# Kernel optimization log

Hardware: AMD Instinct MI355X
Metric: run time of the kernel (lower is better)

The kernel has to match this reference:

```python
import jax, jax.numpy as jnp
import numpy as np

GAMMA = 1.4
N_PTS, N_IC, HID = 32768, 16384, 128


def _mlp(layers, p):
    # tanh MLP; layers = list of (W, b), last layer linear
    h = p
    for W, b in layers[:-1]:
        h = jnp.tanh(h @ W + b)
    W, b = layers[-1]
    return h @ W + b


def setup_inputs() -> dict:
    key = jax.random.key(0)
    ks = jax.random.split(key, 16)
    d = {
        "x_train": jax.random.uniform(ks[0], (N_PTS, 3), jnp.float32),
        "x_initial": jax.random.uniform(ks[1], (N_IC, 3), jnp.float32),
        "ic": jax.random.uniform(ks[2], (4, 4), jnp.float32),
    }
    def lin(k, fi, fo):
        return jax.random.normal(k, (fi, fo), jnp.float32) * np.float32(np.sqrt(1.0 / fi))
    dims_m = [(3, HID), (HID, HID), (HID, HID), (HID, 4)]
    dims_n = [(3, HID), (HID, HID), (HID, HID), (HID, 1)]
    for i, (fi, fo) in enumerate(dims_m):
        d[f"mw{i}"] = lin(ks[3 + i], fi, fo)
        d[f"mb{i}"] = jnp.zeros((fo,), jnp.float32)
    for i, (fi, fo) in enumerate(dims_n):
        d[f"nw{i}"] = lin(ks[8 + i], fi, fo)
        d[f"nb{i}"] = jnp.zeros((fo,), jnp.float32)
    return d


def _loss(x_train, x_initial, ic,
          mw0, mb0, mw1, mb1, mw2, mb2, mw3, mb3,
          nw0, nb0, nw1, nb1, nw2, nb2, nw3, nb3):
    layers_m = [(mw0, mb0), (mw1, mb1), (mw2, mb2), (mw3, mb3)]
    layers_n = [(nw0, nb0), (nw1, nb1), (nw2, nb2), (nw3, nb3)]

    def prim(p):  # p: (3,) = (x, y, t)
        o = _mlp(layers_m, p)
        rho, pr, u, v = o[0], o[1], o[2], o[3]
        E = pr / (GAMMA - 1.0) + 0.5 * rho * (u * u + v * v)
        return rho, pr, u, v, E

    def Ufn(p):  # conserved state U1..U4
        rho, pr, u, v, E = prim(p)
        return jnp.stack([rho, rho * u, rho * v, E])

    def quant(p):  # [U1..U4, f1..f4, g1..g4]
        rho, pr, u, v, E = prim(p)
        U = jnp.stack([rho, rho * u, rho * v, E])
        f = jnp.stack([rho * u, rho * u * u + pr, rho * u * v, u * (E + pr)])
        g = jnp.stack([rho * v, rho * u * v, rho * v * v + pr, v * (E + pr)])
        return jnp.concatenate([U, f, g])

    # one fused forward-mode Jacobian sweep replaces 20 torch autograd.grad calls
    J = jax.vmap(jax.jacfwd(quant))(x_train)            # (N, 12, 3)
    Hs = jax.vmap(jax.jacfwd(jax.jacfwd(Ufn)))(x_train)  # (N, 4, 3, 3)

    mu = 0.01 * jnp.squeeze(_mlp(layers_n, x_train), -1) ** 2  # (N,)
    lap = Hs[:, :, 0, 0] + Hs[:, :, 1, 1]               # U_xx + U_yy, (N, 4)
    # res_i = U_i_t + f_i_x + g_i_y - mu * (U_i_xx + U_i_yy)
    res = J[:, 0:4, 2] + J[:, 4:8, 0] + J[:, 8:12, 1] - mu[:, None] * lap
    r = jnp.mean(res ** 2, axis=0)                      # (4,) -> r1..r4

    # initial-condition quadrant loss (masked means, jit-safe)
    pred = _mlp(layers_m, x_initial)                    # (Ni, 4)
    xl = x_initial[:, 0] < 0.5
    xr = x_initial[:, 0] > 0.5
    yt = x_initial[:, 1] > 0.5
    yb = x_initial[:, 1] < 0.5
    perm = jnp.array([0, 3, 1, 2])  # ic columns -> [rho, p, u, v] target order
    init_loss = jnp.float32(0.0)
    for row, mask in ((1, xl & yt), (3, xr & yt), (0, xl & yb), (2, xr & yb)):
        tgt = ic[row][perm]                             # (4,)
        m = mask.astype(pred.dtype)
        denom = jnp.maximum(jnp.sum(m), 1.0)
        init_loss = init_loss + jnp.sum(m[:, None] * (pred - tgt) ** 2) / denom

    return jnp.sum(r) + 10.0 * init_loss + 0.1 * jnp.mean(mu ** 2)


def reference(x_train, x_initial, ic,
              mw0, mb0, mw1, mb1, mw2, mb2, mw3, mb3,
              nw0, nb0, nw1, nb1, nw2, nb2, nw3, nb3):
    return _loss(x_train, x_initial, ic,
                 mw0, mb0, mw1, mb1, mw2, mb2, mw3, mb3,
                 nw0, nb0, nw1, nb1, nw2, nb2, nw3, nb3)
```

## Files before the change

kernel.cpp:

```cpp
#include <hip/hip_runtime.h>

#define NPTS 32768
#define NIC  16384
#define GRID 256
#define BLK  512
#define NW   8

typedef __attribute__((ext_vector_type(8))) _Float16 f16x8;
typedef __attribute__((ext_vector_type(4))) float f32x4;

#define SWZ(e, r) ((e) ^ (((r) & 7) << 3))
#define MFMA16 __builtin_amdgcn_mfma_f32_16x16x32_f16

__device__ __forceinline__ float tanh_fast(float x) {
    float e = __expf(2.0f * x);
    return 1.0f - 2.0f / (e + 1.0f);
}

__device__ __forceinline__ float wave_allsum(float v) {
#pragma unroll
    for (int off = 32; off > 0; off >>= 1) v += __shfl_xor(v, off, 64);
    return v;
}

__device__ __forceinline__ unsigned short f2hb(float x) {
    return __builtin_bit_cast(unsigned short, (_Float16)x);
}
__device__ __forceinline__ uint2 pack4h(float a, float b, float c, float d) {
    return make_uint2((unsigned)f2hb(a) | ((unsigned)f2hb(b) << 16),
                      (unsigned)f2hb(c) | ((unsigned)f2hb(d) << 16));
}

__global__ __launch_bounds__(BLK) void k_prep(
    const float* __restrict__ mw1, const float* __restrict__ mw2,
    const float* __restrict__ nw1, const float* __restrict__ nw2,
    const float* __restrict__ mw3,
    unsigned short* __restrict__ wt1, unsigned short* __restrict__ wt2,
    unsigned short* __restrict__ nt1, unsigned short* __restrict__ nt2,
    unsigned short* __restrict__ w3t) {
    const int tid = threadIdx.x;
    const int bk = blockIdx.x;
    if (bk == 4) {
        for (int i = tid; i < 2048; i += BLK) w3t[i] = 0;
        __syncthreads();
        if (tid < 512) {
            const int j = tid & 127, k = tid >> 7;
            w3t[k * 128 + SWZ(j, k)] = f2hb(mw3[j * 4 + k]);
        }
        return;
    }
    const float* src = (bk == 0) ? mw1 : (bk == 1) ? mw2 : (bk == 2) ? nw1 : nw2;
    unsigned short* dst = (bk == 0) ? wt1 : (bk == 1) ? wt2 : (bk == 2) ? nt1 : nt2;
    __shared__ float sM[128 * 129];
#pragma unroll
    for (int k = 0; k < 32; k++) {
        const int idx = tid + k * BLK;
        const int j = idx >> 7, n = idx & 127;
        sM[n * 129 + j] = src[idx];
    }
    __syncthreads();
#pragma unroll
    for (int k = 0; k < 32; k++) {
        const int d = tid + k * BLK;
        const int n = d >> 7, js = d & 127;
        const int j = js ^ ((n & 7) << 3);
        dst[d] = f2hb(sM[n * 129 + j]);
    }
}

__global__ __launch_bounds__(BLK) void k_fused(
    const float* __restrict__ xtr, const float* __restrict__ xin,
    const float* __restrict__ icg,
    const float* __restrict__ mw0, const float* __restrict__ mb0,
    const float* __restrict__ mb1, const float* __restrict__ mb2,
    const float* __restrict__ mw3, const float* __restrict__ mb3,
    const float* __restrict__ nw0, const float* __restrict__ nb0,
    const float* __restrict__ nb1, const float* __restrict__ nb2,
    const float* __restrict__ nw3, const float* __restrict__ nb3,
    const unsigned short* __restrict__ wt1, const unsigned short* __restrict__ wt2,
    const unsigned short* __restrict__ nt1, const unsigned short* __restrict__ nt2,
    const unsigned short* __restrict__ w3t,
    float* __restrict__ resPart, float* __restrict__ muPart,
    float* __restrict__ icPart) {
    __shared__ __align__(16) _Float16 sW1[16384];
    __shared__ __align__(16) _Float16 sW2[16384];
    __shared__ __align__(16) _Float16 sH[6 * 4096];
    __shared__ __align__(16) _Float16 sW3[2048];
    __shared__ __align__(16) float sO[768];
    __shared__ float sB[520];
    __shared__ float sV[128];
    __shared__ float sW3v[512];
    __shared__ float sMu[128];
    __shared__ float sTq[16];
    __shared__ float sRed[NW][8];

    const int tid = threadIdx.x;
    const int lane = tid & 63, wv = tid >> 6;
    const int g = lane >> 4, l15 = lane & 15;
    const int rtp = wv >> 1, ptile = wv & 1;
    const int bp = ptile * 16 + l15;
    const int p32 = tid & 31;
    const int chunk = tid >> 5;
    const int base = blockIdx.x * 128;

    {
        const uint4* s4 = (const uint4*)nt1;
        uint4* d4 = (uint4*)sW1;
#pragma unroll
        for (int k = 0; k < 4; k++) d4[tid + k * BLK] = s4[tid + k * BLK];
        s4 = (const uint4*)nt2; d4 = (uint4*)sW2;
#pragma unroll
        for (int k = 0; k < 4; k++) d4[tid + k * BLK] = s4[tid + k * BLK];
        if (tid < 128) {
            sV[tid] = nw3[tid];
            sB[260 + tid] = nb1[tid];
            sB[388 + tid] = nb2[tid];
        }
        if (tid == 0) sB[516] = nb3[0];
    }
    float wxr[8], wyr[8], wzr[8], wbr[8];
#pragma unroll
    for (int j = 0; j < 8; j++) {
        const int n = chunk * 8 + j;
        wxr[j] = nw0[n]; wyr[j] = nw0[128 + n]; wzr[j] = nw0[256 + n]; wbr[j] = nb0[n];
    }
    __syncthreads();

    float accMu2 = 0.f;
    for (int b = 0; b < 4; b++) {
        const int pt0 = base + b * 32;
        {
            const int p = pt0 + p32;
            const float x = xtr[p * 3 + 0], y = xtr[p * 3 + 1], t = xtr[p * 3 + 2];
            float hv[8];
#pragma unroll
            for (int j = 0; j < 8; j++)
                hv[j] = tanh_fast(fmaf(wxr[j], x, fmaf(wyr[j], y, fmaf(wzr[j], t, wbr[j]))));
            const uint2 lo = pack4h(hv[0], hv[1], hv[2], hv[3]);
            const uint2 hi = pack4h(hv[4], hv[5], hv[6], hv[7]);
            *(uint4*)&sH[p32 * 128 + SWZ(chunk * 8, p32)] = make_uint4(lo.x, lo.y, hi.x, hi.y);
        }
        __syncthreads();
#pragma unroll
        for (int L = 0; L < 2; L++) {
            const _Float16* W = (L == 0) ? sW1 : sW2;
            f32x4 a0 = (f32x4){0.f, 0.f, 0.f, 0.f};
            f32x4 a1 = (f32x4){0.f, 0.f, 0.f, 0.f};
#pragma unroll
            for (int ks = 0; ks < 4; ks++) {
                const int ee = SWZ(ks * 32 + g * 8, l15);
                const f16x8 A0 = *(const f16x8*)&W[(rtp * 32 + l15) * 128 + ee];
                const f16x8 A1 = *(const f16x8*)&W[(rtp * 32 + 16 + l15) * 128 + ee];
                const f16x8 Bv = *(const f16x8*)&sH[bp * 128 + ee];
                a0 = MFMA16(A0, Bv, a0, 0, 0, 0);
                a1 = MFMA16(A1, Bv, a1, 0, 0, 0);
            }
            float hv[2][4];
#pragma unroll
            for (int r = 0; r < 4; r++) {
                const int n0 = rtp * 32 + g * 4 + r;
                hv[0][r] = tanh_fast(a0[r] + sB[260 + L * 128 + n0]);
                hv[1][r] = tanh_fast(a1[r] + sB[260 + L * 128 + n0 + 16]);
            }
            __syncthreads();
#pragma unroll
            for (int rr = 0; rr < 2; rr++)
                *(uint2*)&sH[bp * 128 + SWZ(rtp * 32 + rr * 16 + g * 4, bp)] =
                    pack4h(hv[rr][0], hv[rr][1], hv[rr][2], hv[rr][3]);
            __syncthreads();
        }
#pragma unroll
        for (int q = 0; q < 4; q++) {
            const int lp = wv * 4 + q;
            const float h1 = (float)sH[lp * 128 + SWZ(lane, lp)];
            const float h2 = (float)sH[lp * 128 + SWZ(64 + lane, lp)];
            float o = fmaf(h1, sV[lane], h2 * sV[64 + lane]);
            o = wave_allsum(o) + sB[516];
            const float muv = 0.01f * o * o;
            if (lane == 0) sMu[b * 32 + lp] = muv;
            accMu2 += muv * muv;
        }
        __syncthreads();
    }
    if (lane == 0) sRed[wv][0] = accMu2;
    __syncthreads();
    if (tid == 0) {
        float s = 0.f;
#pragma unroll
        for (int w = 0; w < NW; w++) s += sRed[w][0];
        muPart[blockIdx.x] = s;
    }
    __syncthreads();

    {
        const uint4* s4 = (const uint4*)wt1;
        uint4* d4 = (uint4*)sW1;
#pragma unroll
        for (int k = 0; k < 4; k++) d4[tid + k * BLK] = s4[tid + k * BLK];
        s4 = (const uint4*)wt2; d4 = (uint4*)sW2;
#pragma unroll
        for (int k = 0; k < 4; k++) d4[tid + k * BLK] = s4[tid + k * BLK];
        if (tid < 256) ((uint4*)sW3)[tid] = ((const uint4*)w3t)[tid];
        {
            const int k = tid >> 7, j = tid & 127;
            sW3v[k * 128 + j] = mw3[j * 4 + k];
        }
        if (tid < 128) { sB[tid] = mb1[tid]; sB[128 + tid] = mb2[tid]; }
        if (tid < 4) sB[256 + tid] = mb3[tid];
        if (tid < 16) {
            const int k = tid & 3, q = tid >> 2;
            const int row = (q == 0) ? 1 : ((q == 1) ? 3 : ((q == 2) ? 0 : 2));
            const int pc = (k == 0) ? 0 : ((k == 1) ? 3 : ((k == 2) ? 1 : 2));
            sTq[q * 4 + k] = icg[row * 4 + pc];
        }
    }
#pragma unroll
    for (int j = 0; j < 8; j++) {
        const int n = chunk * 8 + j;
        wxr[j] = mw0[n]; wyr[j] = mw0[128 + n]; wzr[j] = mw0[256 + n]; wbr[j] = mb0[n];
    }
    __syncthreads();

    float qs[4] = {0, 0, 0, 0}, qc[4] = {0, 0, 0, 0};
    for (int b = 0; b < 2; b++) {
        const int pt0 = blockIdx.x * 64 + b * 32;
        {
            const int p = pt0 + p32;
            const float x = xin[p * 3 + 0], y = xin[p * 3 + 1], t = xin[p * 3 + 2];
            float hv[8];
#pragma unroll
            for (int j = 0; j < 8; j++)
                hv[j] = tanh_fast(fmaf(wxr[j], x, fmaf(wyr[j], y, fmaf(wzr[j], t, wbr[j]))));
            const uint2 lo = pack4h(hv[0], hv[1], hv[2], hv[3]);
            const uint2 hi = pack4h(hv[4], hv[5], hv[6], hv[7]);
            *(uint4*)&sH[p32 * 128 + SWZ(chunk * 8, p32)] = make_uint4(lo.x, lo.y, hi.x, hi.y);
        }
        __syncthreads();
#pragma unroll
        for (int L = 0; L < 2; L++) {
            const _Float16* W = (L == 0) ? sW1 : sW2;
            f32x4 a0 = (f32x4){0.f, 0.f, 0.f, 0.f};
            f32x4 a1 = (f32x4){0.f, 0.f, 0.f, 0.f};
#pragma unroll
            for (int ks = 0; ks < 4; ks++) {
                const int ee = SWZ(ks * 32 + g * 8, l15);
                const f16x8 A0 = *(const f16x8*)&W[(rtp * 32 + l15) * 128 + ee];
                const f16x8 A1 = *(const f16x8*)&W[(rtp * 32 + 16 + l15) * 128 + ee];
                const f16x8 Bv = *(const f16x8*)&sH[bp * 128 + ee];
                a0 = MFMA16(A0, Bv, a0, 0, 0, 0);
                a1 = MFMA16(A1, Bv, a1, 0, 0, 0);
            }
            float hv[2][4];
#pragma unroll
            for (int r = 0; r < 4; r++) {
                const int n0 = rtp * 32 + g * 4 + r;
                hv[0][r] = tanh_fast(a0[r] + sB[L * 128 + n0]);
                hv[1][r] = tanh_fast(a1[r] + sB[L * 128 + n0 + 16]);
            }
            __syncthreads();
#pragma unroll
            for (int rr = 0; rr < 2; rr++)
                *(uint2*)&sH[bp * 128 + SWZ(rtp * 32 + rr * 16 + g * 4, bp)] =
                    pack4h(hv[rr][0], hv[rr][1], hv[rr][2], hv[rr][3]);
            __syncthreads();
        }
#pragma unroll
        for (int q = 0; q < 4; q++) {
            const int lp = wv * 4 + q;
            const int p = pt0 + lp;
            const float h1 = (float)sH[lp * 128 + SWZ(lane, lp)];
            const float h2 = (float)sH[lp * 128 + SWZ(64 + lane, lp)];
            float o0 = fmaf(h1, sW3v[lane], h2 * sW3v[64 + lane]);
            float o1 = fmaf(h1, sW3v[128 + lane], h2 * sW3v[192 + lane]);
            float o2 = fmaf(h1, sW3v[256 + lane], h2 * sW3v[320 + lane]);
            float o3 = fmaf(h1, sW3v[384 + lane], h2 * sW3v[448 + lane]);
            o0 = wave_allsum(o0) + sB[256];
            o1 = wave_allsum(o1) + sB[257];
            o2 = wave_allsum(o2) + sB[258];
            o3 = wave_allsum(o3) + sB[259];

            const float x = xin[p * 3 + 0];
            const float y = xin[p * 3 + 1];
            int quad = -1;
            if (x < 0.5f && y > 0.5f) quad = 0;
            else if (x > 0.5f && y > 0.5f) quad = 1;
            else if (x < 0.5f && y < 0.5f) quad = 2;
            else if (x > 0.5f && y < 0.5f) quad = 3;
            if (quad >= 0) {
                const float d0 = o0 - sTq[quad * 4 + 0];
                const float d1 = o1 - sTq[quad * 4 + 1];
                const float d2 = o2 - sTq[quad * 4 + 2];
                const float d3 = o3 - sTq[quad * 4 + 3];
                const float ss = d0 * d0 + d1 * d1 + d2 * d2 + d3 * d3;
#pragma unroll
                for (int qq = 0; qq < 4; qq++) {
                    qs[qq] += (quad == qq) ? ss : 0.f;
                    qc[qq] += (quad == qq) ? 1.f : 0.f;
                }
            }
        }
        __syncthreads();
    }
    if (lane == 0) {
#pragma unroll
        for (int q = 0; q < 4; q++) { sRed[wv][q] = qs[q]; sRed[wv][4 + q] = qc[q]; }
    }
    __syncthreads();
    if (tid == 0) {
        float s[8] = {0, 0, 0, 0, 0, 0, 0, 0};
#pragma unroll
        for (int w = 0; w < NW; w++)
#pragma unroll
            for (int q = 0; q < 8; q++) s[q] += sRed[w][q];
#pragma unroll
        for (int q = 0; q < 8; q++) icPart[blockIdx.x * 8 + q] = s[q];
    }
    __syncthreads();

    float racc0 = 0.f, racc1 = 0.f, racc2 = 0.f, racc3 = 0.f;
    for (int b = 0; b < 4; b++) {
        const int pt0 = base + b * 32;

        {
            const int p = pt0 + p32;
            const float x = xtr[p * 3 + 0], y = xtr[p * 3 + 1], t = xtr[p * 3 + 2];
            float ch[6][8];
#pragma unroll
            for (int j = 0; j < 8; j++) {
                const float z = fmaf(wxr[j], x, fmaf(wyr[j], y, fmaf(wzr[j], t, wbr[j])));
                const float a = tanh_fast(z);
                const float s = 1.f - a * a;
                ch[0][j] = a;
                ch[1][j] = s * wxr[j];
                ch[2][j] = s * wyr[j];
                ch[3][j] = s * wzr[j];
                ch[4][j] = -2.f * a * s * wxr[j] * wxr[j];
                ch[5][j] = -2.f * a * s * wyr[j] * wyr[j];
            }
            const int off = p32 * 128 + SWZ(chunk * 8, p32);
#pragma unroll
            for (int c = 0; c < 6; c++) {
                const uint2 lo = pack4h(ch[c][0], ch[c][1], ch[c][2], ch[c][3]);
                const uint2 hi = pack4h(ch[c][4], ch[c][5], ch[c][6], ch[c][7]);
                *(uint4*)&sH[c * 4096 + off] = make_uint4(lo.x, lo.y, hi.x, hi.y);
            }
        }
        __syncthreads();

#pragma unroll
        for (int L = 0; L < 2; L++) {
            const _Float16* W = (L == 0) ? sW1 : sW2;
            f32x4 acc[2][6];
#pragma unroll
            for (int rr = 0; rr < 2; rr++)
#pragma unroll
                for (int c = 0; c < 6; c++) acc[rr][c] = (f32x4){0.f, 0.f, 0.f, 0.f};
#pragma unroll
            for (int ks = 0; ks < 4; ks++) {
                const int ee = SWZ(ks * 32 + g * 8, l15);
                const f16x8 A0 = *(const f16x8*)&W[(rtp * 32 + l15) * 128 + ee];
                const f16x8 A1 = *(const f16x8*)&W[(rtp * 32 + 16 + l15) * 128 + ee];
#pragma unroll
                for (int c = 0; c < 6; c++) {
                    const f16x8 Bv = *(const f16x8*)&sH[c * 4096 + bp * 128 + ee];
                    acc[0][c] = MFMA16(A0, Bv, acc[0][c], 0, 0, 0);
                    acc[1][c] = MFMA16(A1, Bv, acc[1][c], 0, 0, 0);
                }
            }
            float ch[2][6][4];
#pragma unroll
            for (int rr = 0; rr < 2; rr++)
#pragma unroll
                for (int r = 0; r < 4; r++) {
                    const int n = rtp * 32 + rr * 16 + g * 4 + r;
                    const float z0 = acc[rr][0][r] + sB[L * 128 + n];
                    const float a = tanh_fast(z0);
                    const float s = 1.f - a * a;
                    const float zx = acc[rr][1][r], zy = acc[rr][2][r];
                    ch[rr][0][r] = a;
                    ch[rr][1][r] = s * zx;
                    ch[rr][2][r] = s * zy;
                    ch[rr][3][r] = s * acc[rr][3][r];
                    ch[rr][4][r] = s * acc[rr][4][r] - 2.f * a * s * zx * zx;
                    ch[rr][5][r] = s * acc[rr][5][r] - 2.f * a * s * zy * zy;
                }
            __syncthreads();
#pragma unroll
            for (int rr = 0; rr < 2; rr++) {
                const int eo = bp * 128 + SWZ(rtp * 32 + rr * 16 + g * 4, bp);
#pragma unroll
                for (int c = 0; c < 6; c++)
                    *(uint2*)&sH[c * 4096 + eo] =
                        pack4h(ch[rr][c][0], ch[rr][c][1], ch[rr][c][2], ch[rr][c][3]);
            }
            __syncthreads();
        }

#pragma unroll
        for (int tt = 0; tt < 2; tt++) {
            const int t = wv + tt * 8;
            if (t < 12) {
                const int c = t % 6, pti = t / 6;
                const int fp = pti * 16 + l15;
                f32x4 a4 = (f32x4){0.f, 0.f, 0.f, 0.f};
#pragma unroll
                for (int ks = 0; ks < 4; ks++) {
                    const int ee = SWZ(ks * 32 + g * 8, l15);
                    const f16x8 Af = *(const f16x8*)&sW3[l15 * 128 + ee];
                    const f16x8 Bf = *(const f16x8*)&sH[c * 4096 + fp * 128 + ee];
                    a4 = MFMA16(Af, Bf, a4, 0, 0, 0);
                }
                if (g == 0) {
                    float4 o = make_float4(a4[0], a4[1], a4[2], a4[3]);
                    if (c == 0) { o.x += sB[256]; o.y += sB[257]; o.z += sB[258]; o.w += sB[259]; }
                    *(float4*)&sO[(c * 32 + fp) * 4] = o;
                }
            }
        }
        __syncthreads();

        {
            const float m = sMu[b * 32 + p32];
            float oq[4][6];
#pragma unroll
            for (int c = 0; c < 6; c++) {
                const float4 o = *(const float4*)&sO[(c * 32 + p32) * 4];
                oq[0][c] = o.x; oq[1][c] = o.y; oq[2][c] = o.z; oq[3][c] = o.w;
            }
            const float rho = oq[0][0], rho_x = oq[0][1], rho_y = oq[0][2],
                        rho_t = oq[0][3], rho_xx = oq[0][4], rho_yy = oq[0][5];
            const float pr = oq[1][0], pr_x = oq[1][1], pr_y = oq[1][2],
                        pr_t = oq[1][3], pr_xx = oq[1][4], pr_yy = oq[1][5];
            const float u = oq[2][0], u_x = oq[2][1], u_y = oq[2][2],
                        u_t = oq[2][3], u_xx = oq[2][4], u_yy = oq[2][5];
            const float v = oq[3][0], v_x = oq[3][1], v_y = oq[3][2],
                        v_t = oq[3][3], v_xx = oq[3][4], v_yy = oq[3][5];

            const float ig1 = 2.5f;
            const float ke = 0.5f * (u * u + v * v);
            const float E = pr * ig1 + rho * ke;
            const float d_x = u * u_x + v * v_x;
            const float d_y = u * u_y + v * v_y;
            const float d_t = u * u_t + v * v_t;
            const float E_x = pr_x * ig1 + rho_x * ke + rho * d_x;
            const float E_y = pr_y * ig1 + rho_y * ke + rho * d_y;
            const float E_t = pr_t * ig1 + rho_t * ke + rho * d_t;
            const float E_xx = pr_xx * ig1 + rho_xx * ke + 2.f * rho_x * d_x +
                               rho * (u_x * u_x + u * u_xx + v_x * v_x + v * v_xx);
            const float E_yy = pr_yy * ig1 + rho_yy * ke + 2.f * rho_y * d_y +
                               rho * (u_y * u_y + u * u_yy + v_y * v_y + v * v_yy);

            const float r1 = rho_t + (rho_x * u + rho * u_x) + (rho_y * v + rho * v_y)
                           - m * (rho_xx + rho_yy);
            const float r2 = (rho_t * u + rho * u_t)
                           + (rho_x * u * u + 2.f * rho * u * u_x + pr_x)
                           + (rho_y * u * v + rho * u_y * v + rho * u * v_y)
                           - m * ((rho_xx * u + 2.f * rho_x * u_x + rho * u_xx)
                                + (rho_yy * u + 2.f * rho_y * u_y + rho * u_yy));
            const float r3 = (rho_t * v + rho * v_t)
                           + (rho_x * u * v + rho * u_x * v + rho * u * v_x)
                           + (rho_y * v * v + 2.f * rho * v * v_y + pr_y)
                           - m * ((rho_xx * v + 2.f * rho_x * v_x + rho * v_xx)
                                + (rho_yy * v + 2.f * rho_y * v_y + rho * v_yy));
            const float r4 = E_t
                           + (u_x * (E + pr) + u * (E_x + pr_x))
                           + (v_y * (E + pr) + v * (E_y + pr_y))
                           - m * (E_xx + E_yy);
            if (tid < 32) {
                racc0 += r1 * r1; racc1 += r2 * r2;
                racc2 += r3 * r3; racc3 += r4 * r4;
            }
        }
        __syncthreads();
    }

    if (wv == 0) {
        racc0 = wave_allsum(racc0);
        racc1 = wave_allsum(racc1);
        racc2 = wave_allsum(racc2);
        racc3 = wave_allsum(racc3);
        if (lane == 0) {
            resPart[blockIdx.x * 4 + 0] = racc0;
            resPart[blockIdx.x * 4 + 1] = racc1;
            resPart[blockIdx.x * 4 + 2] = racc2;
            resPart[blockIdx.x * 4 + 3] = racc3;
        }
    }
}

__global__ void k_fin(const float* __restrict__ resPart, const float* __restrict__ muPart,
                      const float* __restrict__ icPart, float* __restrict__ out) {
    const int lane = threadIdx.x;
    float r[4] = {0, 0, 0, 0};
    float m2 = 0.f;
    float qs[4] = {0, 0, 0, 0}, qc[4] = {0, 0, 0, 0};
    for (int b = lane; b < GRID; b += 64) {
#pragma unroll
        for (int i = 0; i < 4; i++) r[i] += resPart[b * 4 + i];
        m2 += muPart[b];
#pragma unroll
        for (int q = 0; q < 4; q++) {
            qs[q] += icPart[b * 8 + q];
            qc[q] += icPart[b * 8 + 4 + q];
        }
    }
#pragma unroll
    for (int i = 0; i < 4; i++) r[i] = wave_allsum(r[i]);
    m2 = wave_allsum(m2);
#pragma unroll
    for (int q = 0; q < 4; q++) { qs[q] = wave_allsum(qs[q]); qc[q] = wave_allsum(qc[q]); }
    if (lane == 0) {
        const float sumr = (r[0] + r[1] + r[2] + r[3]) / (float)NPTS;
        float init_loss = 0.f;
#pragma unroll
        for (int q = 0; q < 4; q++) init_loss += qs[q] / fmaxf(qc[q], 1.f);
        out[0] = sumr + 10.f * init_loss + 0.1f * (m2 / (float)NPTS);
    }
}

extern "C" void kernel_launch(void* const* d_in, const int* in_sizes, int n_in,
                              void* d_out, int out_size, void* d_ws, size_t ws_size,
                              hipStream_t stream) {
    const float* xtr = (const float*)d_in[0];
    const float* xin = (const float*)d_in[1];
    const float* icg = (const float*)d_in[2];
    const float* mw0 = (const float*)d_in[3];
    const float* mb0 = (const float*)d_in[4];
    const float* mw1 = (const float*)d_in[5];
    const float* mb1 = (const float*)d_in[6];
    const float* mw2 = (const float*)d_in[7];
    const float* mb2 = (const float*)d_in[8];
    const float* mw3 = (const float*)d_in[9];
    const float* mb3 = (const float*)d_in[10];
    const float* nw0 = (const float*)d_in[11];
    const float* nb0 = (const float*)d_in[12];
    const float* nw1 = (const float*)d_in[13];
    const float* nb1 = (const float*)d_in[14];
    const float* nw2 = (const float*)d_in[15];
    const float* nb2 = (const float*)d_in[16];
    const float* nw3 = (const float*)d_in[17];
    const float* nb3 = (const float*)d_in[18];

    float* wsf = (float*)d_ws;
    float* resPart = wsf;
    float* muPart = wsf + 1024;
    float* icPart = wsf + 1280;
    unsigned short* wt1 = (unsigned short*)(wsf + 3328);
    unsigned short* wt2 = wt1 + 16384;
    unsigned short* nt1 = wt2 + 16384;
    unsigned short* nt2 = nt1 + 16384;
    unsigned short* w3t = nt2 + 16384;

    k_prep<<<5, BLK, 0, stream>>>(mw1, mw2, nw1, nw2, mw3, wt1, wt2, nt1, nt2, w3t);
    k_fused<<<GRID, BLK, 0, stream>>>(xtr, xin, icg,
                                      mw0, mb0, mb1, mb2, mw3, mb3,
                                      nw0, nb0, nb1, nb2, nw3, nb3,
                                      wt1, wt2, nt1, nt2, w3t,
                                      resPart, muPart, icPart);
    k_fin<<<1, 64, 0, stream>>>(resPart, muPart, icPart, (float*)d_out);
}
```

Measured before the change: 66.95 us.

## Stream single weight buffer via async global-to-LDS loads with 256-thread blocks

Halves the block to 256 threads and replaces the two resident weight matrices with one LDS weight buffer. The next layer's fp16 weights are prefetched with global_load_lds while the current layer's tanh and derivative epilogue runs. It also moves the viscosity-net output layer onto MFMA and cuts LDS footprint so more blocks can fit per CU. The cost is that weights are re-streamed from global/L2 for every layer and every tile, with extra barriers and vmcnt waits, and the residual stage now runs on only one wave.

```diff
diff --git a/kernel.cpp b/kernel.cpp
--- a/kernel.cpp
+++ b/kernel.cpp
@@ -3,14 +3,15 @@
 #define NPTS 32768
 #define NIC  16384
 #define GRID 256
-#define BLK  512
-#define NW   8
+#define BLK  256
+#define NW   4
 
 typedef __attribute__((ext_vector_type(8))) _Float16 f16x8;
 typedef __attribute__((ext_vector_type(4))) float f32x4;
 
 #define SWZ(e, r) ((e) ^ (((r) & 7) << 3))
 #define MFMA16 __builtin_amdgcn_mfma_f32_16x16x32_f16
+#define VMCNT0 asm volatile("s_waitcnt vmcnt(0)" ::: "memory")
 
 __device__ __forceinline__ float tanh_fast(float x) {
     float e = __expf(2.0f * x);
@@ -31,7 +32,20 @@
                       (unsigned)f2hb(c) | ((unsigned)f2hb(d) << 16));
 }
 
-__global__ __launch_bounds__(BLK) void k_prep(
+__device__ __forceinline__ void stage_w_async(const unsigned short* __restrict__ src,
+                                              _Float16* dst, int tid) {
+    const unsigned int* gp = (const unsigned int*)src;
+    unsigned int* lp = (unsigned int*)dst;
+#pragma unroll
+    for (int k = 0; k < 8; k++) {
+        __builtin_amdgcn_global_load_lds(
+            (const __attribute__((address_space(1))) unsigned int*)(gp + (tid + k * BLK) * 4),
+            (__attribute__((address_space(3))) unsigned int*)(lp + (tid + k * BLK) * 4),
+            16, 0, 0);
+    }
+}
+
+__global__ __launch_bounds__(512) void k_prep(
     const float* __restrict__ mw1, const float* __restrict__ mw2,
     const float* __restrict__ nw1, const float* __restrict__ nw2,
     const float* __restrict__ mw3,
@@ -41,7 +55,7 @@
     const int tid = threadIdx.x;
     const int bk = blockIdx.x;
     if (bk == 4) {
-        for (int i = tid; i < 2048; i += BLK) w3t[i] = 0;
+        for (int i = tid; i < 2048; i += 512) w3t[i] = 0;
         __syncthreads();
         if (tid < 512) {
             const int j = tid & 127, k = tid >> 7;
@@ -54,17 +68,110 @@
     __shared__ float sM[128 * 129];
 #pragma unroll
     for (int k = 0; k < 32; k++) {
-        const int idx = tid + k * BLK;
+        const int idx = tid + k * 512;
         const int j = idx >> 7, n = idx & 127;
         sM[n * 129 + j] = src[idx];
     }
     __syncthreads();
 #pragma unroll
     for (int k = 0; k < 32; k++) {
-        const int d = tid + k * BLK;
+        const int d = tid + k * 512;
         const int n = d >> 7, js = d & 127;
         const int j = js ^ ((n & 7) << 3);
         dst[d] = f2hb(sM[n * 129 + j]);
+    }
+}
+
+__device__ __forceinline__ void hidden_val(const _Float16* sW, _Float16* sHv,
+                                           const float* bias,
+                                           const unsigned short* nextW, _Float16* sWdst,
+                                           int tid, int wv, int g, int l15) {
+    f32x4 acc[2][4];
+#pragma unroll
+    for (int rr = 0; rr < 2; rr++)
+#pragma unroll
+        for (int pt = 0; pt < 4; pt++) acc[rr][pt] = (f32x4){0.f, 0.f, 0.f, 0.f};
+#pragma unroll
+    for (int ks = 0; ks < 4; ks++) {
+        const int ee = SWZ(ks * 32 + g * 8, l15);
+        const f16x8 A0 = *(const f16x8*)&sW[(wv * 32 + l15) * 128 + ee];
+        const f16x8 A1 = *(const f16x8*)&sW[(wv * 32 + 16 + l15) * 128 + ee];
+#pragma unroll
+        for (int pt = 0; pt < 4; pt++) {
+            const f16x8 Bv = *(const f16x8*)&sHv[(pt * 16 + l15) * 128 + ee];
+            acc[0][pt] = MFMA16(A0, Bv, acc[0][pt], 0, 0, 0);
+            acc[1][pt] = MFMA16(A1, Bv, acc[1][pt], 0, 0, 0);
+        }
+    }
+    __syncthreads();
+    if (nextW) stage_w_async(nextW, sWdst, tid);
+    float hv[2][4][4];
+#pragma unroll
+    for (int rr = 0; rr < 2; rr++)
+#pragma unroll
+        for (int pt = 0; pt < 4; pt++)
+#pragma unroll
+            for (int r = 0; r < 4; r++) {
+                const int n = wv * 32 + rr * 16 + g * 4 + r;
+                hv[rr][pt][r] = tanh_fast(acc[rr][pt][r] + bias[n]);
+            }
+#pragma unroll
+    for (int rr = 0; rr < 2; rr++)
+#pragma unroll
+        for (int pt = 0; pt < 4; pt++) {
+            const int row = pt * 16 + l15;
+            *(uint2*)&sHv[row * 128 + SWZ(wv * 32 + rr * 16 + g * 4, row)] =
+                pack4h(hv[rr][pt][0], hv[rr][pt][1], hv[rr][pt][2], hv[rr][pt][3]);
+        }
+}
+
+__device__ __forceinline__ void hidden_res(const _Float16* sW, _Float16* sH6,
+                                           const float* bias,
+                                           const unsigned short* nextW, _Float16* sWdst,
+                                           int tid, int wv, int g, int l15) {
+    f32x4 acc[2][6];
+#pragma unroll
+    for (int rr = 0; rr < 2; rr++)
+#pragma unroll
+        for (int c = 0; c < 6; c++) acc[rr][c] = (f32x4){0.f, 0.f, 0.f, 0.f};
+#pragma unroll
+    for (int ks = 0; ks < 4; ks++) {
+        const int ee = SWZ(ks * 32 + g * 8, l15);
+        const f16x8 A0 = *(const f16x8*)&sW[(wv * 32 + l15) * 128 + ee];
+        const f16x8 A1 = *(const f16x8*)&sW[(wv * 32 + 16 + l15) * 128 + ee];
+#pragma unroll
+        for (int c = 0; c < 6; c++) {
+            const f16x8 Bv = *(const f16x8*)&sH6[c * 2048 + l15 * 128 + ee];
+            acc[0][c] = MFMA16(A0, Bv, acc[0][c], 0, 0, 0);
+            acc[1][c] = MFMA16(A1, Bv, acc[1][c], 0, 0, 0);
+        }
+    }
+    __syncthreads();
+    if (nextW) stage_w_async(nextW, sWdst, tid);
+    float ch[2][6][4];
+#pragma unroll
+    for (int rr = 0; rr < 2; rr++)
+#pragma unroll
+        for (int r = 0; r < 4; r++) {
+            const int n = wv * 32 + rr * 16 + g * 4 + r;
+            const float z0 = acc[rr][0][r] + bias[n];
+            const float a = tanh_fast(z0);
+            const float s = 1.f - a * a;
+            const float zx = acc[rr][1][r], zy = acc[rr][2][r];
+            ch[rr][0][r] = a;
+            ch[rr][1][r] = s * zx;
+            ch[rr][2][r] = s * zy;
+            ch[rr][3][r] = s * acc[rr][3][r];
+            ch[rr][4][r] = s * acc[rr][4][r] - 2.f * a * s * zx * zx;
+            ch[rr][5][r] = s * acc[rr][5][r] - 2.f * a * s * zy * zy;
+        }
+#pragma unroll
+    for (int rr = 0; rr < 2; rr++) {
+        const int eo = l15 * 128 + SWZ(wv * 32 + rr * 16 + g * 4, l15);
+#pragma unroll
+        for (int c = 0; c < 6; c++)
+            *(uint2*)&sH6[c * 2048 + eo] =
+                pack4h(ch[rr][c][0], ch[rr][c][1], ch[rr][c][2], ch[rr][c][3]);
     }
 }
 
@@ -73,7 +180,7 @@
     const float* __restrict__ icg,
     const float* __restrict__ mw0, const float* __restrict__ mb0,
     const float* __restrict__ mb1, const float* __restrict__ mb2,
-    const float* __restrict__ mw3, const float* __restrict__ mb3,
+    const float* __restrict__ mb3,
     const float* __restrict__ nw0, const float* __restrict__ nb0,
     const float* __restrict__ nb1, const float* __restrict__ nb2,
     const float* __restrict__ nw3, const float* __restrict__ nb3,
@@ -82,14 +189,11 @@
     const unsigned short* __restrict__ w3t,
     float* __restrict__ resPart, float* __restrict__ muPart,
     float* __restrict__ icPart) {
-    __shared__ __align__(16) _Float16 sW1[16384];
-    __shared__ __align__(16) _Float16 sW2[16384];
-    __shared__ __align__(16) _Float16 sH[6 * 4096];
-    __shared__ __align__(16) _Float16 sW3[2048];
-    __shared__ __align__(16) float sO[768];
+    __shared__ __align__(16) _Float16 sW[16384];
+    __shared__ __align__(16) _Float16 sH[6 * 2048];
+    __shared__ __align__(16) _Float16 sA[2048];
+    __shared__ __align__(16) float sO[384];
     __shared__ float sB[520];
-    __shared__ float sV[128];
-    __shared__ float sW3v[512];
     __shared__ float sMu[128];
     __shared__ float sTq[16];
     __shared__ float sRed[NW][8];
@@ -97,40 +201,36 @@
     const int tid = threadIdx.x;
     const int lane = tid & 63, wv = tid >> 6;
     const int g = lane >> 4, l15 = lane & 15;
-    const int rtp = wv >> 1, ptile = wv & 1;
-    const int bp = ptile * 16 + l15;
-    const int p32 = tid & 31;
-    const int chunk = tid >> 5;
-    const int base = blockIdx.x * 128;
-
-    {
-        const uint4* s4 = (const uint4*)nt1;
-        uint4* d4 = (uint4*)sW1;
-#pragma unroll
-        for (int k = 0; k < 4; k++) d4[tid + k * BLK] = s4[tid + k * BLK];
-        s4 = (const uint4*)nt2; d4 = (uint4*)sW2;
-#pragma unroll
-        for (int k = 0; k < 4; k++) d4[tid + k * BLK] = s4[tid + k * BLK];
-        if (tid < 128) {
-            sV[tid] = nw3[tid];
-            sB[260 + tid] = nb1[tid];
-            sB[388 + tid] = nb2[tid];
-        }
-        if (tid == 0) sB[516] = nb3[0];
-    }
+    const int p16 = tid & 15, chunk = tid >> 4;
+
+    stage_w_async(nt1, sW, tid);
+    if (tid < 128) { sB[tid] = mb1[tid]; sB[260 + tid] = nb1[tid]; }
+    else           { sB[tid] = mb2[tid - 128]; sB[260 + tid] = nb2[tid - 128]; }
+    if (tid < 4) sB[256 + tid] = mb3[tid];
+    if (tid == 4) sB[516] = nb3[0];
+    if (tid < 16) {
+        const int k = tid & 3, q = tid >> 2;
+        const int row = (q == 0) ? 1 : ((q == 1) ? 3 : ((q == 2) ? 0 : 2));
+        const int pc = (k == 0) ? 0 : ((k == 1) ? 3 : ((k == 2) ? 1 : 2));
+        sTq[q * 4 + k] = icg[row * 4 + pc];
+    }
+    for (int i = tid; i < 2048; i += BLK) sA[i] = (_Float16)0.f;
+    if (tid < 128) sA[tid] = (_Float16)nw3[tid];
+
     float wxr[8], wyr[8], wzr[8], wbr[8];
 #pragma unroll
     for (int j = 0; j < 8; j++) {
         const int n = chunk * 8 + j;
         wxr[j] = nw0[n]; wyr[j] = nw0[128 + n]; wzr[j] = nw0[256 + n]; wbr[j] = nb0[n];
     }
-    __syncthreads();
 
     float accMu2 = 0.f;
-    for (int b = 0; b < 4; b++) {
-        const int pt0 = base + b * 32;
-        {
-            const int p = pt0 + p32;
+    for (int bt = 0; bt < 2; bt++) {
+        const int pt0 = blockIdx.x * 128 + bt * 64;
+        const int ee0 = SWZ(chunk * 8, p16);
+#pragma unroll
+        for (int pp = 0; pp < 4; pp++) {
+            const int p = pt0 + pp * 16 + p16;
             const float x = xtr[p * 3 + 0], y = xtr[p * 3 + 1], t = xtr[p * 3 + 2];
             float hv[8];
 #pragma unroll
@@ -138,94 +238,49 @@
                 hv[j] = tanh_fast(fmaf(wxr[j], x, fmaf(wyr[j], y, fmaf(wzr[j], t, wbr[j]))));
             const uint2 lo = pack4h(hv[0], hv[1], hv[2], hv[3]);
             const uint2 hi = pack4h(hv[4], hv[5], hv[6], hv[7]);
-            *(uint4*)&sH[p32 * 128 + SWZ(chunk * 8, p32)] = make_uint4(lo.x, lo.y, hi.x, hi.y);
-        }
-        __syncthreads();
-#pragma unroll
-        for (int L = 0; L < 2; L++) {
-            const _Float16* W = (L == 0) ? sW1 : sW2;
-            f32x4 a0 = (f32x4){0.f, 0.f, 0.f, 0.f};
-            f32x4 a1 = (f32x4){0.f, 0.f, 0.f, 0.f};
+            *(uint4*)&sH[(pp * 16 + p16) * 128 + ee0] = make_uint4(lo.x, lo.y, hi.x, hi.y);
+        }
+        VMCNT0; __syncthreads();
+        hidden_val(sW, sH, &sB[260], nt2, sW, tid, wv, g, l15);
+        VMCNT0; __syncthreads();
+        hidden_val(sW, sH, &sB[388], (bt == 0) ? nt1 : wt1, sW, tid, wv, g, l15);
+        __syncthreads();
+        {
+            f32x4 a4 = (f32x4){0.f, 0.f, 0.f, 0.f};
 #pragma unroll
             for (int ks = 0; ks < 4; ks++) {
                 const int ee = SWZ(ks * 32 + g * 8, l15);
-                const f16x8 A0 = *(const f16x8*)&W[(rtp * 32 + l15) * 128 + ee];
-                const f16x8 A1 = *(const f16x8*)&W[(rtp * 32 + 16 + l15) * 128 + ee];
-                const f16x8 Bv = *(const f16x8*)&sH[bp * 128 + ee];
-                a0 = MFMA16(A0, Bv, a0, 0, 0, 0);
-                a1 = MFMA16(A1, Bv, a1, 0, 0, 0);
-            }
-            float hv[2][4];
-#pragma unroll
-            for (int r = 0; r < 4; r++) {
-                const int n0 = rtp * 32 + g * 4 + r;
-                hv[0][r] = tanh_fast(a0[r] + sB[260 + L * 128 + n0]);
-                hv[1][r] = tanh_fast(a1[r] + sB[260 + L * 128 + n0 + 16]);
-            }
-            __syncthreads();
-#pragma unroll
-            for (int rr = 0; rr < 2; rr++)
-                *(uint2*)&sH[bp * 128 + SWZ(rtp * 32 + rr * 16 + g * 4, bp)] =
-                    pack4h(hv[rr][0], hv[rr][1], hv[rr][2], hv[rr][3]);
-            __syncthreads();
-        }
-#pragma unroll
-        for (int q = 0; q < 4; q++) {
-            const int lp = wv * 4 + q;
-            const float h1 = (float)sH[lp * 128 + SWZ(lane, lp)];
-            const float h2 = (float)sH[lp * 128 + SWZ(64 + lane, lp)];
-            float o = fmaf(h1, sV[lane], h2 * sV[64 + lane]);
-            o = wave_allsum(o) + sB[516];
-            const float muv = 0.01f * o * o;
-            if (lane == 0) sMu[b * 32 + lp] = muv;
-            accMu2 += muv * muv;
-        }
-        __syncthreads();
-    }
+                const f16x8 Af = *(const f16x8*)&sA[l15 * 128 + ee];
+                const f16x8 Bv = *(const f16x8*)&sH[(wv * 16 + l15) * 128 + ee];
+                a4 = MFMA16(Af, Bv, a4, 0, 0, 0);
+            }
+            if (g == 0) {
+                const float o = a4[0] + sB[516];
+                const float muv = 0.01f * o * o;
+                sMu[bt * 64 + wv * 16 + l15] = muv;
+                accMu2 += muv * muv;
+            }
+        }
+        __syncthreads();
+    }
+    accMu2 = wave_allsum(accMu2);
     if (lane == 0) sRed[wv][0] = accMu2;
     __syncthreads();
-    if (tid == 0) {
-        float s = 0.f;
-#pragma unroll
-        for (int w = 0; w < NW; w++) s += sRed[w][0];
-        muPart[blockIdx.x] = s;
-    }
-    __syncthreads();
-
-    {
-        const uint4* s4 = (const uint4*)wt1;
-        uint4* d4 = (uint4*)sW1;
-#pragma unroll
-        for (int k = 0; k < 4; k++) d4[tid + k * BLK] = s4[tid + k * BLK];
-        s4 = (const uint4*)wt2; d4 = (uint4*)sW2;
-#pragma unroll
-        for (int k = 0; k < 4; k++) d4[tid + k * BLK] = s4[tid + k * BLK];
-        if (tid < 256) ((uint4*)sW3)[tid] = ((const uint4*)w3t)[tid];
-        {
-            const int k = tid >> 7, j = tid & 127;
-            sW3v[k * 128 + j] = mw3[j * 4 + k];
-        }
-        if (tid < 128) { sB[tid] = mb1[tid]; sB[128 + tid] = mb2[tid]; }
-        if (tid < 4) sB[256 + tid] = mb3[tid];
-        if (tid < 16) {
-            const int k = tid & 3, q = tid >> 2;
-            const int row = (q == 0) ? 1 : ((q == 1) ? 3 : ((q == 2) ? 0 : 2));
-            const int pc = (k == 0) ? 0 : ((k == 1) ? 3 : ((k == 2) ? 1 : 2));
-            sTq[q * 4 + k] = icg[row * 4 + pc];
-        }
-    }
+    if (tid == 0)
+        muPart[blockIdx.x] = sRed[0][0] + sRed[1][0] + sRed[2][0] + sRed[3][0];
+
 #pragma unroll
     for (int j = 0; j < 8; j++) {
         const int n = chunk * 8 + j;
         wxr[j] = mw0[n]; wyr[j] = mw0[128 + n]; wzr[j] = mw0[256 + n]; wbr[j] = mb0[n];
     }
-    __syncthreads();
-
-    float qs[4] = {0, 0, 0, 0}, qc[4] = {0, 0, 0, 0};
-    for (int b = 0; b < 2; b++) {
-        const int pt0 = blockIdx.x * 64 + b * 32;
-        {
-            const int p = pt0 + p32;
+
+    {
+        const int pt0 = blockIdx.x * 64;
+        const int ee0 = SWZ(chunk * 8, p16);
+#pragma unroll
+        for (int pp = 0; pp < 4; pp++) {
+            const int p = pt0 + pp * 16 + p16;
             const float x = xin[p * 3 + 0], y = xin[p * 3 + 1], t = xin[p * 3 + 2];
             float hv[8];
 #pragma unroll
@@ -233,96 +288,77 @@
                 hv[j] = tanh_fast(fmaf(wxr[j], x, fmaf(wyr[j], y, fmaf(wzr[j], t, wbr[j]))));
             const uint2 lo = pack4h(hv[0], hv[1], hv[2], hv[3]);
             const uint2 hi = pack4h(hv[4], hv[5], hv[6], hv[7]);
-            *(uint4*)&sH[p32 * 128 + SWZ(chunk * 8, p32)] = make_uint4(lo.x, lo.y, hi.x, hi.y);
-        }
-        __syncthreads();
-#pragma unroll
-        for (int L = 0; L < 2; L++) {
-            const _Float16* W = (L == 0) ? sW1 : sW2;
-            f32x4 a0 = (f32x4){0.f, 0.f, 0.f, 0.f};
-            f32x4 a1 = (f32x4){0.f, 0.f, 0.f, 0.f};
+            *(uint4*)&sH[(pp * 16 + p16) * 128 + ee0] = make_uint4(lo.x, lo.y, hi.x, hi.y);
+        }
+        VMCNT0; __syncthreads();
+        hidden_val(sW, sH, &sB[0], wt2, sW, tid, wv, g, l15);
+        ((uint4*)sA)[tid] = ((const uint4*)w3t)[tid];
+        VMCNT0; __syncthreads();
+        hidden_val(sW, sH, &sB[128], wt1, sW, tid, wv, g, l15);
+        __syncthreads();
+        float qs[4] = {0, 0, 0, 0}, qc[4] = {0, 0, 0, 0};
+        {
+            f32x4 a4 = (f32x4){0.f, 0.f, 0.f, 0.f};
 #pragma unroll
             for (int ks = 0; ks < 4; ks++) {
                 const int ee = SWZ(ks * 32 + g * 8, l15);
-                const f16x8 A0 = *(const f16x8*)&W[(rtp * 32 + l15) * 128 + ee];
-                const f16x8 A1 = *(const f16x8*)&W[(rtp * 32 + 16 + l15) * 128 + ee];
-                const f16x8 Bv = *(const f16x8*)&sH[bp * 128 + ee];
-                a0 = MFMA16(A0, Bv, a0, 0, 0, 0);
-                a1 = MFMA16(A1, Bv, a1, 0, 0, 0);
-            }
-            float hv[2][4];
-#pragma unroll
-            for (int r = 0; r < 4; r++) {
-                const int n0 = rtp * 32 + g * 4 + r;
-                hv[0][r] = tanh_fast(a0[r] + sB[L * 128 + n0]);
-                hv[1][r] = tanh_fast(a1[r] + sB[L * 128 + n0 + 16]);
-            }
-            __syncthreads();
-#pragma unroll
-            for (int rr = 0; rr < 2; rr++)
-                *(uint2*)&sH[bp * 128 + SWZ(rtp * 32 + rr * 16 + g * 4, bp)] =
-                    pack4h(hv[rr][0], hv[rr][1], hv[rr][2], hv[rr][3]);
-            __syncthreads();
-        }
-#pragma unroll
-        for (int q = 0; q < 4; q++) {
-            const int lp = wv * 4 + q;
-            const int p = pt0 + lp;
-            const float h1 = (float)sH[lp * 128 + SWZ(lane, lp)];
-            const float h2 = (float)sH[lp * 128 + SWZ(64 + lane, lp)];
-            float o0 = fmaf(h1, sW3v[lane], h2 * sW3v[64 + lane]);
-            float o1 = fmaf(h1, sW3v[128 + lane], h2 * sW3v[192 + lane]);
-            float o2 = fmaf(h1, sW3v[256 + lane], h2 * sW3v[320 + lane]);
-            float o3 = fmaf(h1, sW3v[384 + lane], h2 * sW3v[448 + lane]);
-            o0 = wave_allsum(o0) + sB[256];
-            o1 = wave_allsum(o1) + sB[257];
-            o2 = wave_allsum(o2) + sB[258];
-            o3 = wave_allsum(o3) + sB[259];
-
-            const float x = xin[p * 3 + 0];
-            const float y = xin[p * 3 + 1];
-            int quad = -1;
-            if (x < 0.5f && y > 0.5f) quad = 0;
-            else if (x > 0.5f && y > 0.5f) quad = 1;
-            else if (x < 0.5f && y < 0.5f) quad = 2;
-            else if (x > 0.5f && y < 0.5f) quad = 3;
-            if (quad >= 0) {
-                const float d0 = o0 - sTq[quad * 4 + 0];
-                const float d1 = o1 - sTq[quad * 4 + 1];
-                const float d2 = o2 - sTq[quad * 4 + 2];
-                const float d3 = o3 - sTq[quad * 4 + 3];
-                const float ss = d0 * d0 + d1 * d1 + d2 * d2 + d3 * d3;
-#pragma unroll
-                for (int qq = 0; qq < 4; qq++) {
-                    qs[qq] += (quad == qq) ? ss : 0.f;
-                    qc[qq] += (quad == qq) ? 1.f : 0.f;
+                const f16x8 Af = *(const f16x8*)&sA[l15 * 128 + ee];
+                const f16x8 Bv = *(const f16x8*)&sH[(wv * 16 + l15) * 128 + ee];
+                a4 = MFMA16(Af, Bv, a4, 0, 0, 0);
+            }
+            if (g == 0) {
+                const int p = pt0 + wv * 16 + l15;
+                const float o0 = a4[0] + sB[256];
+                const float o1 = a4[1] + sB[257];
+                const float o2 = a4[2] + sB[258];
+                const float o3 = a4[3] + sB[259];
+                const float x = xin[p * 3 + 0];
+                const float y = xin[p * 3 + 1];
+                int quad = -1;
+                if (x < 0.5f && y > 0.5f) quad = 0;
+                else if (x > 0.5f && y > 0.5f) quad = 1;
+                else if (x < 0.5f && y < 0.5f) quad = 2;
+                else if (x > 0.5f && y < 0.5f) quad = 3;
+                if (quad >= 0) {
+                    const float d0 = o0 - sTq[quad * 4 + 0];
+                    const float d1 = o1 - sTq[quad * 4 + 1];
+                    const float d2 = o2 - sTq[quad * 4 + 2];
+                    const float d3 = o3 - sTq[quad * 4 + 3];
+                    const float ss = d0 * d0 + d1 * d1 + d2 * d2 + d3 * d3;
+#pragma unroll
+                    for (int qq = 0; qq < 4; qq++) {
+                        qs[qq] += (quad == qq) ? ss : 0.f;
+                        qc[qq] += (quad == qq) ? 1.f : 0.f;
+                    }
                 }
             }
         }
         __syncthreads();
-    }
-    if (lane == 0) {
-#pragma unroll
-        for (int q = 0; q < 4; q++) { sRed[wv][q] = qs[q]; sRed[wv][4 + q] = qc[q]; }
-    }
-    __syncthreads();
-    if (tid == 0) {
-        float s[8] = {0, 0, 0, 0, 0, 0, 0, 0};
-#pragma unroll
-        for (int w = 0; w < NW; w++)
-#pragma unroll
-            for (int q = 0; q < 8; q++) s[q] += sRed[w][q];
-#pragma unroll
-        for (int q = 0; q < 8; q++) icPart[blockIdx.x * 8 + q] = s[q];
-    }
-    __syncthreads();
+#pragma unroll
+        for (int qq = 0; qq < 4; qq++) {
+            qs[qq] = wave_allsum(qs[qq]);
+            qc[qq] = wave_allsum(qc[qq]);
+        }
+        if (lane == 0) {
+#pragma unroll
+            for (int qq = 0; qq < 4; qq++) { sRed[wv][qq] = qs[qq]; sRed[wv][4 + qq] = qc[qq]; }
+        }
+        __syncthreads();
+        if (tid == 0) {
+#pragma unroll
+            for (int q = 0; q < 8; q++)
+                icPart[blockIdx.x * 8 + q] =
+                    sRed[0][q] + sRed[1][q] + sRed[2][q] + sRed[3][q];
+        }
+        __syncthreads();
+    }
 
     float racc0 = 0.f, racc1 = 0.f, racc2 = 0.f, racc3 = 0.f;
-    for (int b = 0; b < 4; b++) {
-        const int pt0 = base + b * 32;
-
+    const int base = blockIdx.x * 128;
+    for (int b = 0; b < 8; b++) {
+        const int pt0 = base + b * 16;
         {
-            const int p = pt0 + p32;
+            const int p = pt0 + p16;
             const float x = xtr[p * 3 + 0], y = xtr[p * 3 + 1], t = xtr[p * 3 + 2];
             float ch[6][8];
 #pragma unroll
@@ -337,94 +373,47 @@
                 ch[4][j] = -2.f * a * s * wxr[j] * wxr[j];
                 ch[5][j] = -2.f * a * s * wyr[j] * wyr[j];
             }
-            const int off = p32 * 128 + SWZ(chunk * 8, p32);
+            const int off = p16 * 128 + SWZ(chunk * 8, p16);
 #pragma unroll
             for (int c = 0; c < 6; c++) {
                 const uint2 lo = pack4h(ch[c][0], ch[c][1], ch[c][2], ch[c][3]);
                 const uint2 hi = pack4h(ch[c][4], ch[c][5], ch[c][6], ch[c][7]);
-                *(uint4*)&sH[c * 4096 + off] = make_uint4(lo.x, lo.y, hi.x, hi.y);
-            }
-        }
-        __syncthreads();
-
-#pragma unroll
-        for (int L = 0; L < 2; L++) {
-            const _Float16* W = (L == 0) ? sW1 : sW2;
-            f32x4 acc[2][6];
-#pragma unroll
-            for (int rr = 0; rr < 2; rr++)
-#pragma unroll
-                for (int c = 0; c < 6; c++) acc[rr][c] = (f32x4){0.f, 0.f, 0.f, 0.f};
-#pragma unroll
-            for (int ks = 0; ks < 4; ks++) {
-                const int ee = SWZ(ks * 32 + g * 8, l15);
-                const f16x8 A0 = *(const f16x8*)&W[(rtp * 32 + l15) * 128 + ee];
-                const f16x8 A1 = *(const f16x8*)&W[(rtp * 32 + 16 + l15) * 128 + ee];
-#pragma unroll
-                for (int c = 0; c < 6; c++) {
-                    const f16x8 Bv = *(const f16x8*)&sH[c * 4096 + bp * 128 + ee];
-                    acc[0][c] = MFMA16(A0, Bv, acc[0][c], 0, 0, 0);
-                    acc[1][c] = MFMA16(A1, Bv, acc[1][c], 0, 0, 0);
-                }
-            }
-            float ch[2][6][4];
-#pragma unroll
-            for (int rr = 0; rr < 2; rr++)
-#pragma unroll
-                for (int r = 0; r < 4; r++) {
-                    const int n = rtp * 32 + rr * 16 + g * 4 + r;
-                    const float z0 = acc[rr][0][r] + sB[L * 128 + n];
-                    const float a = tanh_fast(z0);
-                    const float s = 1.f - a * a;
-                    const float zx = acc[rr][1][r], zy = acc[rr][2][r];
-                    ch[rr][0][r] = a;
-                    ch[rr][1][r] = s * zx;
-                    ch[rr][2][r] = s * zy;
-                    ch[rr][3][r] = s * acc[rr][3][r];
-                    ch[rr][4][r] = s * acc[rr][4][r] - 2.f * a * s * zx * zx;
-                    ch[rr][5][r] = s * acc[rr][5][r] - 2.f * a * s * zy * zy;
-                }
-            __syncthreads();
-#pragma unroll
-            for (int rr = 0; rr < 2; rr++) {
-                const int eo = bp * 128 + SWZ(rtp * 32 + rr * 16 + g * 4, bp);
-#pragma unroll
-                for (int c = 0; c < 6; c++)
-                    *(uint2*)&sH[c * 4096 + eo] =
-                        pack4h(ch[rr][c][0], ch[rr][c][1], ch[rr][c][2], ch[rr][c][3]);
-            }
-            __syncthreads();
-        }
-
+                *(uint4*)&sH[c * 2048 + off] = make_uint4(lo.x, lo.y, hi.x, hi.y);
+            }
+        }
+        VMCNT0; __syncthreads();
+        hidden_res(sW, sH, &sB[0], wt2, sW, tid, wv, g, l15);
+        VMCNT0; __syncthreads();
+        hidden_res(sW, sH, &sB[128],
+                   (b < 7) ? wt1 : (const unsigned short*)nullptr, sW, tid, wv, g, l15);
+        __syncthreads();
 #pragma unroll
         for (int tt = 0; tt < 2; tt++) {
-            const int t = wv + tt * 8;
-            if (t < 12) {
-                const int c = t % 6, pti = t / 6;
-                const int fp = pti * 16 + l15;
+            const int c = wv + tt * 4;
+            if (c < 6) {
                 f32x4 a4 = (f32x4){0.f, 0.f, 0.f, 0.f};
 #pragma unroll
                 for (int ks = 0; ks < 4; ks++) {
                     const int ee = SWZ(ks * 32 + g * 8, l15);
-                    const f16x8 Af = *(const f16x8*)&sW3[l15 * 128 + ee];
-                    const f16x8 Bf = *(const f16x8*)&sH[c * 4096 + fp * 128 + ee];
+                    const f16x8 Af = *(const f16x8*)&sA[l15 * 128 + ee];
+                    const f16x8 Bf = *(const f16x8*)&sH[c * 2048 + l15 * 128 + ee];
                     a4 = MFMA16(Af, Bf, a4, 0, 0, 0);
                 }
                 if (g == 0) {
                     float4 o = make_float4(a4[0], a4[1], a4[2], a4[3]);
                     if (c == 0) { o.x += sB[256]; o.y += sB[257]; o.z += sB[258]; o.w += sB[259]; }
-                    *(float4*)&sO[(c * 32 + fp) * 4] = o;
+                    *(float4*)&sO[(c * 16 + l15) * 4] = o;
                 }
             }
         }
         __syncthreads();
-
-        {
-            const float m = sMu[b * 32 + p32];
+        if (wv == 0) {
+            const int pp = lane & 15;
+            const float m = sMu[b * 16 + pp];
             float oq[4][6];
 #pragma unroll
             for (int c = 0; c < 6; c++) {
-                const float4 o = *(const float4*)&sO[(c * 32 + p32) * 4];
+                const float4 o = *(const float4*)&sO[(c * 16 + pp) * 4];
                 oq[0][c] = o.x; oq[1][c] = o.y; oq[2][c] = o.z; oq[3][c] = o.w;
             }
             const float rho = oq[0][0], rho_x = oq[0][1], rho_y = oq[0][2],
@@ -466,7 +455,7 @@
                            + (u_x * (E + pr) + u * (E_x + pr_x))
                            + (v_y * (E + pr) + v * (E_y + pr_y))
                            - m * (E_xx + E_yy);
-            if (tid < 32) {
+            if (lane < 16) {
                 racc0 += r1 * r1; racc1 += r2 * r2;
                 racc2 += r3 * r3; racc3 += r4 * r4;
             }
@@ -551,9 +540,9 @@
     unsigned short* nt2 = nt1 + 16384;
     unsigned short* w3t = nt2 + 16384;
 
-    k_prep<<<5, BLK, 0, stream>>>(mw1, mw2, nw1, nw2, mw3, wt1, wt2, nt1, nt2, w3t);
+    k_prep<<<5, 512, 0, stream>>>(mw1, mw2, nw1, nw2, mw3, wt1, wt2, nt1, nt2, w3t);
     k_fused<<<GRID, BLK, 0, stream>>>(xtr, xin, icg,
-                                      mw0, mb0, mb1, mb2, mw3, mb3,
+                                      mw0, mb0, mb1, mb2, mb3,
                                       nw0, nb0, nb1, nb2, nw3, nb3,
                                       wt1, wt2, nt1, nt2, w3t,
                                       resPart, muPart, icPart);
```

New measurement: 70.18 us. 4.8% more time.
